# Performance work log

Measured on AMD Instinct MI355X. Metric: run time of the kernel, lower is better.

Reference implementation:

```python
import jax, jax.numpy as jnp
import numpy as np

NUM_CLASSES = 80
SCORE_THRESH = 0.5
NMS_THRESH = 0.5
TOP_K = 200  # max candidates kept per (image, class) before greedy NMS


def setup_inputs() -> dict:
    key = jax.random.key(0)
    k1, k2, k3 = jax.random.split(key, 3)
    B, A, HW, C = 8, 3, 5776, NUM_CLASSES  # 608-input YOLOv4 P3 level: 76*76
    # well-formed boxes in [0,1]: x1y1 + positive wh
    xy = jax.random.uniform(k1, (B, A, HW, 2)) * 0.8
    wh = jax.random.uniform(k2, (B, A, HW, 2)) * 0.2 + 0.01
    boxes = jnp.concatenate([xy, xy + wh], axis=-1)
    scores = jax.random.uniform(k3, (B, A, HW, C))
    return {"boxes": boxes, "scores": scores}


def _pairwise_iou(b):
    # b: [K, 4] (x1, y1, x2, y2) -> IoU matrix [K, K] (union mode)
    x1, y1, x2, y2 = b[:, 0], b[:, 1], b[:, 2], b[:, 3]
    area = (x2 - x1) * (y2 - y1)
    xx1 = jnp.maximum(x1[:, None], x1[None, :])
    yy1 = jnp.maximum(y1[:, None], y1[None, :])
    xx2 = jnp.minimum(x2[:, None], x2[None, :])
    yy2 = jnp.minimum(y2[:, None], y2[None, :])
    inter = jnp.maximum(0.0, xx2 - xx1) * jnp.maximum(0.0, yy2 - yy1)
    return inter / (area[:, None] + area[None, :] - inter)


def _nms_one(boxes, scores):
    # boxes: [N, 4], scores: [N] -> top-K candidates with greedy-NMS keep mask
    s = jnp.where(scores > SCORE_THRESH, scores, -jnp.inf)  # score threshold filter
    top_s, idx = jax.lax.top_k(s, TOP_K)                    # descending, like argsort()[::-1]
    b = boxes[idx]                                          # [K, 4]
    valid = jnp.isfinite(top_s)
    iou = _pairwise_iou(b)                                  # [K, K]

    def body(keep, i):
        # if box i survives, suppress all lower-scored boxes with IoU > thresh
        sup = keep[i] & (iou[i] > NMS_THRESH) & (jnp.arange(TOP_K) > i)
        return keep & ~sup, None

    keep, _ = jax.lax.scan(body, valid, jnp.arange(TOP_K))
    return b, top_s, keep


def reference(boxes, scores):
    B, A, HW, _ = boxes.shape
    C = scores.shape[-1]
    b = boxes.reshape(B, A * HW, 4)
    s = scores.reshape(B, A * HW, C)
    per_img = jax.vmap(lambda bb, ss: jax.vmap(_nms_one, in_axes=(None, 1))(bb, ss))
    boxes_k, scores_k, keep = per_img(b, s)  # [B,C,K,4], [B,C,K], [B,C,K]
    cls = jnp.broadcast_to(jnp.arange(C, dtype=boxes.dtype)[None, :, None], keep.shape)
    out_box = jnp.where(keep[..., None], boxes_k, 0.0)
    out_score = jnp.where(keep, scores_k, 0.0)
    out_cls = jnp.where(keep, cls, 0.0)
    # padded detections [B, C, K, 6] = (x1, y1, x2, y2, score, class_id)
    return jnp.concatenate([out_box, out_score[..., None], out_cls[..., None]], axis=-1)
```

## Files before the change

### kernel.cpp

```cpp
#include <hip/hip_runtime.h>
#include <stdint.h>

#define B_IMG  8
#define NANCH  17328
#define NCLS   80
#define TOPK   200
#define NTHR   256
#define NTHRB  512
#define CHUNK  64
#define NCHK   ((NANCH + CHUNK - 1) / CHUNK)
#define NCHKP  272
#define SLOT   12
#define NPOS   (NCHK * SLOT)
#define NBC    (B_IMG * NCLS)
#define THRESH_HI 0.98f

__device__ __forceinline__ void hist_add(float s, unsigned int* hist) {
  if (s > 0.5f) {
    unsigned int bin = (__float_as_uint(s) - 0x3F000000u) >> 15;
    if (bin > 255u) bin = 255u;
    atomicAdd(&hist[bin], 1u);
  }
}

__global__ __launch_bounds__(NTHR) void scatter_k(
    const float* __restrict__ scores,
    unsigned char* __restrict__ cnt2,
    unsigned long long* __restrict__ cand) {
  const int nb = blockIdx.x;
  const int b  = blockIdx.y;
  const int tid = threadIdx.x;
  const int wv = tid >> 6, lane = tid & 63;
  const int n0 = nb * CHUNK;

  __shared__ float tile[CHUNK][81];

  const int nrow = (NANCH - n0 < CHUNK) ? (NANCH - n0) : CHUNK;
  const int nf4 = nrow * (NCLS / 4);
  const float4* src4 = (const float4*)(scores + (size_t)(b * NANCH + n0) * NCLS);
  for (int f = tid; f < nf4; f += NTHR) {
    float4 v = src4[f];
    int n = f / 20, c4 = (f - n * 20) * 4;
    tile[n][c4] = v.x; tile[n][c4 + 1] = v.y;
    tile[n][c4 + 2] = v.z; tile[n][c4 + 3] = v.w;
  }
  __syncthreads();

  const bool rv = (lane < nrow);
  const unsigned long long lt = (1ull << lane) - 1ull;
  const int cbase = wv * 20;
#pragma unroll 4
  for (int cc = 0; cc < 20; ++cc) {
    const int c = cbase + cc;
    const int bc = b * NCLS + c;
    float s = rv ? tile[lane][c] : 0.f;
    const bool cd = (s > THRESH_HI);
    unsigned long long bal = __ballot(cd);
    if (cd) {
      unsigned int r = (unsigned int)__popcll(bal & lt);
      if (r < SLOT)
        cand[((size_t)bc * NCHK + nb) * SLOT + r] =
            ((unsigned long long)__float_as_uint(s) << 32) |
            (unsigned long long)(0xFFFFFFFFu - (unsigned int)(n0 + lane));
    }
    if (lane == 0)
      cnt2[(size_t)bc * NCHKP + nb] = (unsigned char)__popcll(bal);
  }
}

__global__ __launch_bounds__(NTHRB) void backend_k(
    const float* __restrict__ scores, const float* __restrict__ boxes,
    const unsigned char* __restrict__ cnt2, const unsigned long long* __restrict__ cand,
    float* __restrict__ out) {
  const int bc = blockIdx.x;
  const int b = bc / NCLS;
  const int c = bc - b * NCLS;
  const int tid = threadIdx.x;
  const int wv = tid >> 6, lane = tid & 63;
  const unsigned long long lt = (1ull << lane) - 1ull;

  __shared__ unsigned long long selk[512];
  __shared__ unsigned long long sorted[256];
  __shared__ unsigned int hist[256];
  __shared__ float sx1[256], sy1[256], sx2[256], sy2[256], sar[256], ssc[256];
  __shared__ int skeep[256];
  __shared__ __align__(16) unsigned long long sup[TOPK][4];
  __shared__ __align__(16) float eout[TOPK * 6];
  __shared__ unsigned int sh_cutbits;
  __shared__ int sh_sel, sh_bad;

  if (tid < 256) sorted[tid] = 0ull;
  if (tid == 0) { sh_sel = 0; sh_bad = 0; }
  __syncthreads();

  const unsigned long long* cb0 = cand + (size_t)bc * NCHK * SLOT;
  const unsigned char* ct0 = cnt2 + (size_t)bc * NCHKP;
  for (int p = tid; p < NPOS; p += NTHRB) {
    const int ch = p / SLOT;
    const int sl = p - ch * SLOT;
    unsigned int ci = (unsigned int)ct0[ch];
    if (sl == 0 && ci > SLOT) sh_bad = 1;
    unsigned long long k = 0ull;
    bool pred = (sl < (int)ci);
    if (pred) k = cb0[p];
    unsigned long long bal = __ballot(pred);
    if (bal) {
      int base0 = 0;
      if (lane == 0) base0 = atomicAdd(&sh_sel, (int)__popcll(bal));
      base0 = __shfl(base0, 0, 64);
      if (pred) {
        int pos = base0 + (int)__popcll(bal & lt);
        if (pos < 512) selk[pos] = k;
      }
    }
  }
  __syncthreads();

  int Msel = sh_sel;
  const bool fb = (sh_bad != 0) || (Msel < TOPK) || (Msel > 512);

  if (fb) {
    if (tid < 256) hist[tid] = 0u;
    if (tid == 0) sh_sel = 0;
    __syncthreads();
    const float* src = scores + (size_t)b * NANCH * NCLS + c;
    for (int i = tid; i < NANCH; i += NTHRB) hist_add(src[(size_t)i * NCLS], hist);
    __syncthreads();
    if (tid == 0) {
      unsigned int acc = 0;
      int cut = 0;
      for (int bin = 255; bin >= 0; --bin) {
        acc += hist[bin];
        if (acc >= TOPK) { cut = bin; break; }
      }
      sh_cutbits = 0x3F000000u + ((unsigned int)cut << 15);
    }
    __syncthreads();
    const unsigned int cutbits = sh_cutbits;
    for (int i = tid; i < NANCH; i += NTHRB) {
      float s = src[(size_t)i * NCLS];
      if (s > 0.5f && __float_as_uint(s) >= cutbits) {
        int slot = atomicAdd(&sh_sel, 1);
        if (slot < 512)
          selk[slot] = ((unsigned long long)__float_as_uint(s) << 32) |
                       (unsigned long long)(0xFFFFFFFFu - (unsigned int)i);
      }
    }
    __syncthreads();
    Msel = sh_sel; if (Msel > 512) Msel = 512;
  }

  if (tid < Msel) {
    const unsigned long long mk = selk[tid];
    int r = 0;
#pragma unroll 8
    for (int j = 0; j < Msel; ++j) r += (selk[j] > mk) ? 1 : 0;
    if (r < 256) sorted[r] = mk;
  }
  __syncthreads();

  if (tid < 256) {
    unsigned long long key = sorted[tid];
    int valid = (tid < TOPK) && (key != 0ull);
    unsigned int idx = 0xFFFFFFFFu - (unsigned int)(key & 0xFFFFFFFFull);
    float4 bx = make_float4(0.f, 0.f, 0.f, 0.f);
    if (valid) bx = ((const float4*)boxes)[(size_t)b * NANCH + idx];
    sx1[tid] = bx.x; sy1[tid] = bx.y; sx2[tid] = bx.z; sy2[tid] = bx.w;
    sar[tid] = __fmul_rn(bx.z - bx.x, bx.w - bx.y);
    ssc[tid] = valid ? __uint_as_float((unsigned int)(key >> 32)) : 0.f;
    skeep[tid] = valid;
  }
  __syncthreads();

  {
    float jx1[4], jy1[4], jx2[4], jy2[4], ja[4];
#pragma unroll
    for (int r = 0; r < 4; ++r) {
      int j = (r << 6) | lane;
      jx1[r] = sx1[j]; jy1[r] = sy1[j]; jx2[r] = sx2[j]; jy2[r] = sy2[j];
      ja[r] = sar[j];
    }
    float nx1 = sx1[wv], ny1 = sy1[wv], nx2 = sx2[wv], ny2 = sy2[wv], na = sar[wv];
    for (int k = 0; k < 25; ++k) {
      const int i = (k << 3) + wv;
      const float xi1 = nx1, yi1 = ny1, xi2 = nx2, yi2 = ny2, ai = na;
      const int inx = i + 8;
      if (inx < TOPK) {
        nx1 = sx1[inx]; ny1 = sy1[inx]; nx2 = sx2[inx]; ny2 = sy2[inx];
        na = sar[inx];
      }
      const int d = i >> 6;
      const int il = i & 63;
      unsigned long long dmask = (il == 63) ? 0ull : ((~0ull) << (il + 1));
      if (d == 3) dmask &= 0xFFull;
      unsigned long long w[4];
#pragma unroll
      for (int r = 0; r < 4; ++r) {
        unsigned long long word = 0ull;
        if ((r << 6) + 63 > i) {
          const unsigned long long wmask =
              (r > d) ? ((r == 3) ? 0xFFull : ~0ull) : dmask;
          float xx1 = fmaxf(xi1, jx1[r]);
          float yy1 = fmaxf(yi1, jy1[r]);
          float xx2 = fminf(xi2, jx2[r]);
          float yy2 = fminf(yi2, jy2[r]);
          float iw = fmaxf(0.f, __fsub_rn(xx2, xx1));
          float ih = fmaxf(0.f, __fsub_rn(yy2, yy1));
          float inter = __fmul_rn(iw, ih);
          float denom = __fsub_rn(__fadd_rn(ai, ja[r]), inter);
          float q = __fmul_rn(inter, __builtin_amdgcn_rcpf(denom));
          word = __ballot(q > 0.5f);
          unsigned long long gb = __ballot(fabsf(q - 0.5f) < 1e-5f) & wmask;
          if (gb)
            word = __ballot(__fdiv_rn(inter, denom) > 0.5f);
          word &= wmask;
        }
        w[r] = word;
      }
      if (lane == 0) {
        ulonglong2* dst = (ulonglong2*)&sup[i][0];
        ulonglong2 t0; t0.x = w[0]; t0.y = w[1];
        ulonglong2 t1; t1.x = w[2]; t1.y = w[3];
        dst[0] = t0; dst[1] = t1;
      }
    }
  }
  __syncthreads();

  if (tid < 64) {
    unsigned long long k0 = __ballot(skeep[tid] != 0);
    unsigned long long k1 = __ballot(skeep[64 + tid] != 0);
    unsigned long long k2 = __ballot(skeep[128 + tid] != 0);
    unsigned long long k3 = __ballot(skeep[192 + tid] != 0);
#define NMS_SCAN_WORD(KW, BASE, CNT)                                     \
    _Pragma("unroll 8")                                                  \
    for (int li = 0; li < (CNT); ++li) {                                 \
      const ulonglong2* s2p =                                            \
          reinterpret_cast<const ulonglong2*>(&sup[(BASE) + li][0]);     \
      ulonglong2 sa = s2p[0];                                            \
      ulonglong2 sb = s2p[1];                                            \
      unsigned long long m = 0ull - ((KW >> li) & 1ull);                 \
      k0 &= ~(sa.x & m); k1 &= ~(sa.y & m);                              \
      k2 &= ~(sb.x & m); k3 &= ~(sb.y & m);                              \
    }
    NMS_SCAN_WORD(k0, 0, 64)
    NMS_SCAN_WORD(k1, 64, 64)
    NMS_SCAN_WORD(k2, 128, 64)
    NMS_SCAN_WORD(k3, 192, 8)
#undef NMS_SCAN_WORD
    skeep[tid]        = (int)((k0 >> tid) & 1ull);
    skeep[64 + tid]   = (int)((k1 >> tid) & 1ull);
    skeep[128 + tid]  = (int)((k2 >> tid) & 1ull);
    skeep[192 + tid]  = (int)((k3 >> tid) & 1ull);
  }
  __syncthreads();

  if (tid < TOPK) {
    int kp = skeep[tid];
    eout[tid * 6 + 0] = kp ? sx1[tid] : 0.f;
    eout[tid * 6 + 1] = kp ? sy1[tid] : 0.f;
    eout[tid * 6 + 2] = kp ? sx2[tid] : 0.f;
    eout[tid * 6 + 3] = kp ? sy2[tid] : 0.f;
    eout[tid * 6 + 4] = kp ? ssc[tid] : 0.f;
    eout[tid * 6 + 5] = kp ? (float)c : 0.f;
  }
  __syncthreads();

  float4* out4 = (float4*)(out + (size_t)bc * (TOPK * 6));
  const float4* e4 = (const float4*)eout;
  for (int f = tid; f < (TOPK * 6) / 4; f += NTHRB) out4[f] = e4[f];
}

__global__ __launch_bounds__(NTHR) void select_nms_k(
    const float* __restrict__ boxes, const float* __restrict__ scores,
    float* __restrict__ out) {
  const int blk = blockIdx.x;
  const int b = blk / NCLS;
  const int c = blk - b * NCLS;
  const int tid = threadIdx.x;

  __shared__ unsigned int hist[256];
  __shared__ unsigned long long keys[1024];
  __shared__ float sx1[TOPK], sy1[TOPK], sx2[TOPK], sy2[TOPK], sar[TOPK], ssc[TOPK];
  __shared__ int skeep[TOPK];
  __shared__ unsigned int sh_cutbits;
  __shared__ int sh_m;

  const float* src = scores + (size_t)b * NANCH * NCLS + c;

  for (int j = tid; j < 256; j += NTHR) hist[j] = 0;
  if (tid == 0) sh_m = 0;
  __syncthreads();

  for (int i = tid; i < NANCH; i += NTHR) hist_add(src[(size_t)i * NCLS], hist);
  __syncthreads();

  if (tid == 0) {
    unsigned int acc = 0;
    int cut = 0;
    for (int bin = 255; bin >= 0; --bin) {
      acc += hist[bin];
      if (acc >= TOPK) { cut = bin; break; }
    }
    sh_cutbits = 0x3F000000u + ((unsigned int)cut << 15);
  }
  __syncthreads();
  const unsigned int cutbits = sh_cutbits;

  for (int i = tid; i < NANCH; i += NTHR) {
    float s = src[(size_t)i * NCLS];
    if (s > 0.5f && __float_as_uint(s) >= cutbits) {
      int slot = atomicAdd(&sh_m, 1);
      if (slot < 1024)
        keys[slot] = ((unsigned long long)__float_as_uint(s) << 32) |
                     (unsigned long long)(0xFFFFFFFFu - (unsigned int)i);
    }
  }
  __syncthreads();
  int M = sh_m; if (M > 1024) M = 1024;
  for (int j = M + tid; j < 1024; j += NTHR) keys[j] = 0ull;

  for (int size = 2; size <= 1024; size <<= 1) {
    for (int st = size >> 1; st > 0; st >>= 1) {
      __syncthreads();
      for (int t = tid; t < 512; t += NTHR) {
        int lo = 2 * t - (t & (st - 1));
        int hi = lo + st;
        bool desc = ((lo & size) == 0);
        unsigned long long a = keys[lo], bb = keys[hi];
        if ((a < bb) == desc) { keys[lo] = bb; keys[hi] = a; }
      }
    }
  }
  __syncthreads();

  if (tid < TOPK) {
    unsigned long long key = keys[tid];
    int valid = (key != 0ull);
    float sc = __uint_as_float((unsigned int)(key >> 32));
    unsigned int idx = 0xFFFFFFFFu - (unsigned int)(key & 0xFFFFFFFFull);
    float4 bx = make_float4(0.f, 0.f, 0.f, 0.f);
    if (valid) bx = ((const float4*)boxes)[(size_t)b * NANCH + idx];
    sx1[tid] = bx.x; sy1[tid] = bx.y; sx2[tid] = bx.z; sy2[tid] = bx.w;
    sar[tid] = __fmul_rn(bx.z - bx.x, bx.w - bx.y);
    ssc[tid] = valid ? sc : 0.f;
    skeep[tid] = valid;
  }
  __syncthreads();

  if (tid < 64) {
    const int lane = tid;
    float x1v[4], y1v[4], x2v[4], y2v[4], av[4];
    int km = 0;
#pragma unroll
    for (int r = 0; r < 4; ++r) {
      int j = lane + (r << 6);
      if (j < TOPK) {
        x1v[r] = sx1[j]; y1v[r] = sy1[j]; x2v[r] = sx2[j]; y2v[r] = sy2[j];
        av[r] = sar[j];
        if (skeep[j]) km |= (1 << r);
      } else {
        x1v[r] = 0.f; y1v[r] = 0.f; x2v[r] = 0.f; y2v[r] = 0.f; av[r] = 0.f;
      }
    }
#pragma unroll
    for (int ri = 0; ri < 4; ++ri) {
      const int imax = (ri == 3) ? (TOPK - 192) : 64;
      for (int li = 0; li < imax; ++li) {
        const int i = (ri << 6) + li;
        int kmi = __shfl(km, li, 64);
        if (!((kmi >> ri) & 1)) continue;
        float xi1 = __shfl(x1v[ri], li, 64);
        float yi1 = __shfl(y1v[ri], li, 64);
        float xi2 = __shfl(x2v[ri], li, 64);
        float yi2 = __shfl(y2v[ri], li, 64);
        float ai  = __shfl(av[ri],  li, 64);
#pragma unroll
        for (int r = 0; r < 4; ++r) {
          int j = lane + (r << 6);
          if (j > i && j < TOPK && ((km >> r) & 1)) {
            float xx1 = fmaxf(xi1, x1v[r]);
            float yy1 = fmaxf(yi1, y1v[r]);
            float xx2 = fminf(xi2, x2v[r]);
            float yy2 = fminf(yi2, y2v[r]);
            float iw = fmaxf(0.f, __fsub_rn(xx2, xx1));
            float ih = fmaxf(0.f, __fsub_rn(yy2, yy1));
            float inter = __fmul_rn(iw, ih);
            float denom = __fsub_rn(__fadd_rn(ai, av[r]), inter);
            float iou = __fdiv_rn(inter, denom);
            if (iou > 0.5f) km &= ~(1 << r);
          }
        }
      }
    }
#pragma unroll
    for (int r = 0; r < 4; ++r) {
      int j = lane + (r << 6);
      if (j < TOPK) skeep[j] = (km >> r) & 1;
    }
  }
  __syncthreads();

  const size_t base = ((size_t)b * NCLS + c) * (TOPK * 6);
  for (int f = tid; f < TOPK * 6; f += NTHR) {
    int k = f / 6, comp = f - k * 6;
    float v = 0.f;
    if (skeep[k]) {
      switch (comp) {
        case 0: v = sx1[k]; break;
        case 1: v = sy1[k]; break;
        case 2: v = sx2[k]; break;
        case 3: v = sy2[k]; break;
        case 4: v = ssc[k]; break;
        default: v = (float)c; break;
      }
    }
    out[base + f] = v;
  }
}

extern "C" void kernel_launch(void* const* d_in, const int* in_sizes, int n_in,
                              void* d_out, int out_size, void* d_ws, size_t ws_size,
                              hipStream_t stream) {
  (void)in_sizes; (void)n_in; (void)out_size;
  const float* boxes  = (const float*)d_in[0];
  const float* scores = (const float*)d_in[1];
  float* out = (float*)d_out;

  const size_t need_c2 = (size_t)NBC * NCHKP;
  const size_t need_cd = (size_t)NBC * NCHK * SLOT * sizeof(uint64_t);
  const size_t need = need_c2 + need_cd;

  if (ws_size >= need) {
    char* w = (char*)d_ws;
    unsigned char* cnt2      = (unsigned char*)w;       w += need_c2;
    unsigned long long* cand = (unsigned long long*)w;

    scatter_k<<<dim3(NCHK, B_IMG), NTHR, 0, stream>>>(scores, cnt2, cand);
    backend_k<<<NBC, NTHRB, 0, stream>>>(scores, boxes, cnt2, cand, out);
  } else {
    select_nms_k<<<NBC, NTHR, 0, stream>>>(boxes, scores, out);
  }
}
```

Baseline: 72.95 us.

## Split backend into select and NMS kernels with bitonic sort and division-free IoU test

New measurement: 79.71 us. +9.3%, slower.

```diff
diff --git a/kernel.cpp b/kernel.cpp
--- a/kernel.cpp
+++ b/kernel.cpp
@@ -68,34 +68,28 @@
   }
 }
 
-__global__ __launch_bounds__(NTHRB) void backend_k(
+__global__ __launch_bounds__(NTHR) void select_k(
     const float* __restrict__ scores, const float* __restrict__ boxes,
     const unsigned char* __restrict__ cnt2, const unsigned long long* __restrict__ cand,
-    float* __restrict__ out) {
+    float4* __restrict__ stagedBox, unsigned long long* __restrict__ stagedKey) {
   const int bc = blockIdx.x;
   const int b = bc / NCLS;
   const int c = bc - b * NCLS;
   const int tid = threadIdx.x;
-  const int wv = tid >> 6, lane = tid & 63;
+  const int lane = tid & 63;
   const unsigned long long lt = (1ull << lane) - 1ull;
 
   __shared__ unsigned long long selk[512];
-  __shared__ unsigned long long sorted[256];
   __shared__ unsigned int hist[256];
-  __shared__ float sx1[256], sy1[256], sx2[256], sy2[256], sar[256], ssc[256];
-  __shared__ int skeep[256];
-  __shared__ __align__(16) unsigned long long sup[TOPK][4];
-  __shared__ __align__(16) float eout[TOPK * 6];
   __shared__ unsigned int sh_cutbits;
   __shared__ int sh_sel, sh_bad;
 
-  if (tid < 256) sorted[tid] = 0ull;
   if (tid == 0) { sh_sel = 0; sh_bad = 0; }
   __syncthreads();
 
   const unsigned long long* cb0 = cand + (size_t)bc * NCHK * SLOT;
   const unsigned char* ct0 = cnt2 + (size_t)bc * NCHKP;
-  for (int p = tid; p < NPOS; p += NTHRB) {
+  for (int p = tid; p < NPOS; p += NTHR) {
     const int ch = p / SLOT;
     const int sl = p - ch * SLOT;
     unsigned int ci = (unsigned int)ct0[ch];
@@ -124,7 +118,7 @@
     if (tid == 0) sh_sel = 0;
     __syncthreads();
     const float* src = scores + (size_t)b * NANCH * NCLS + c;
-    for (int i = tid; i < NANCH; i += NTHRB) hist_add(src[(size_t)i * NCLS], hist);
+    for (int i = tid; i < NANCH; i += NTHR) hist_add(src[(size_t)i * NCLS], hist);
     __syncthreads();
     if (tid == 0) {
       unsigned int acc = 0;
@@ -137,7 +131,7 @@
     }
     __syncthreads();
     const unsigned int cutbits = sh_cutbits;
-    for (int i = tid; i < NANCH; i += NTHRB) {
+    for (int i = tid; i < NANCH; i += NTHR) {
       float s = src[(size_t)i * NCLS];
       if (s > 0.5f && __float_as_uint(s) >= cutbits) {
         int slot = atomicAdd(&sh_sel, 1);
@@ -150,21 +144,51 @@
     Msel = sh_sel; if (Msel > 512) Msel = 512;
   }
 
-  if (tid < Msel) {
-    const unsigned long long mk = selk[tid];
-    int r = 0;
-#pragma unroll 8
-    for (int j = 0; j < Msel; ++j) r += (selk[j] > mk) ? 1 : 0;
-    if (r < 256) sorted[r] = mk;
-  }
-  __syncthreads();
-
-  if (tid < 256) {
-    unsigned long long key = sorted[tid];
+  const int S = (Msel <= 256) ? 256 : 512;
+  for (int j = Msel + tid; j < S; j += NTHR) selk[j] = 0ull;
+
+  for (int size = 2; size <= S; size <<= 1) {
+    for (int st = size >> 1; st > 0; st >>= 1) {
+      __syncthreads();
+      for (int t = tid; t < (S >> 1); t += NTHR) {
+        int lo = 2 * t - (t & (st - 1));
+        int hi = lo + st;
+        bool desc = ((lo & size) == 0);
+        unsigned long long a = selk[lo], bb = selk[hi];
+        if ((a < bb) == desc) { selk[lo] = bb; selk[hi] = a; }
+      }
+    }
+  }
+  __syncthreads();
+
+  {
+    unsigned long long key = selk[tid];
     int valid = (tid < TOPK) && (key != 0ull);
     unsigned int idx = 0xFFFFFFFFu - (unsigned int)(key & 0xFFFFFFFFull);
     float4 bx = make_float4(0.f, 0.f, 0.f, 0.f);
     if (valid) bx = ((const float4*)boxes)[(size_t)b * NANCH + idx];
+    stagedBox[(size_t)bc * 256 + tid] = bx;
+    stagedKey[(size_t)bc * 256 + tid] = valid ? key : 0ull;
+  }
+}
+
+__global__ __launch_bounds__(NTHRB) void nms_k(
+    const float4* __restrict__ stagedBox, const unsigned long long* __restrict__ stagedKey,
+    float* __restrict__ out) {
+  const int bc = blockIdx.x;
+  const int c = bc - (bc / NCLS) * NCLS;
+  const int tid = threadIdx.x;
+  const int wv = tid >> 6, lane = tid & 63;
+
+  __shared__ float sx1[256], sy1[256], sx2[256], sy2[256], sar[256], ssc[256];
+  __shared__ int skeep[256];
+  __shared__ __align__(16) unsigned long long sup[TOPK][4];
+  __shared__ __align__(16) float eout[TOPK * 6];
+
+  if (tid < 256) {
+    unsigned long long key = stagedKey[(size_t)bc * 256 + tid];
+    float4 bx = stagedBox[(size_t)bc * 256 + tid];
+    int valid = (tid < TOPK) && (key != 0ull);
     sx1[tid] = bx.x; sy1[tid] = bx.y; sx2[tid] = bx.z; sy2[tid] = bx.w;
     sar[tid] = __fmul_rn(bx.z - bx.x, bx.w - bx.y);
     ssc[tid] = valid ? __uint_as_float((unsigned int)(key >> 32)) : 0.f;
@@ -208,9 +232,11 @@
           float ih = fmaxf(0.f, __fsub_rn(yy2, yy1));
           float inter = __fmul_rn(iw, ih);
           float denom = __fsub_rn(__fadd_rn(ai, ja[r]), inter);
-          float q = __fmul_rn(inter, __builtin_amdgcn_rcpf(denom));
-          word = __ballot(q > 0.5f);
-          unsigned long long gb = __ballot(fabsf(q - 0.5f) < 1e-5f) & wmask;
+          float i2 = __fadd_rn(inter, inter);
+          word = __ballot(i2 > denom);
+          unsigned long long gb =
+              __ballot((i2 > denom) &&
+                       (i2 <= __fmul_rn(denom, 1.0000005f))) & wmask;
           if (gb)
             word = __ballot(__fdiv_rn(inter, denom) > 0.5f);
           word &= wmask;
@@ -429,15 +455,21 @@
 
   const size_t need_c2 = (size_t)NBC * NCHKP;
   const size_t need_cd = (size_t)NBC * NCHK * SLOT * sizeof(uint64_t);
-  const size_t need = need_c2 + need_cd;
+  const size_t need_sb = (size_t)NBC * 256 * sizeof(float4);
+  const size_t need_sk = (size_t)NBC * 256 * sizeof(uint64_t);
+  const size_t need = need_c2 + need_cd + need_sb + need_sk;
 
   if (ws_size >= need) {
     char* w = (char*)d_ws;
-    unsigned char* cnt2      = (unsigned char*)w;       w += need_c2;
-    unsigned long long* cand = (unsigned long long*)w;
+    unsigned char* cnt2           = (unsigned char*)w;       w += need_c2;
+    unsigned long long* cand      = (unsigned long long*)w;  w += need_cd;
+    float4* stagedBox             = (float4*)w;              w += need_sb;
+    unsigned long long* stagedKey = (unsigned long long*)w;
 
     scatter_k<<<dim3(NCHK, B_IMG), NTHR, 0, stream>>>(scores, cnt2, cand);
-    backend_k<<<NBC, NTHRB, 0, stream>>>(scores, boxes, cnt2, cand, out);
+    select_k<<<NBC, NTHR, 0, stream>>>(scores, boxes, cnt2, cand,
+                                       stagedBox, stagedKey);
+    nms_k<<<NBC, NTHRB, 0, stream>>>(stagedBox, stagedKey, out);
   } else {
     select_nms_k<<<NBC, NTHR, 0, stream>>>(boxes, scores, out);
   }
```

## Fuse IoU computation into serial NMS scan, bitonic sort, and 256-thread backend

Applied to the files above, without the earlier changes.

Result: slower. 98.53 us (+35.1%).

```diff
diff --git a/kernel.cpp b/kernel.cpp
--- a/kernel.cpp
+++ b/kernel.cpp
@@ -6,7 +6,6 @@
 #define NCLS   80
 #define TOPK   200
 #define NTHR   256
-#define NTHRB  512
 #define CHUNK  64
 #define NCHK   ((NANCH + CHUNK - 1) / CHUNK)
 #define NCHKP  272
@@ -68,7 +67,35 @@
   }
 }
 
-__global__ __launch_bounds__(NTHRB) void backend_k(
+#define DO_R(R, KR, EXTRA) {                                                  \
+    bool mk = (EXTRA);                                                        \
+    float xx1 = fmaxf(xi1, jx1[R]);                                           \
+    float yy1 = fmaxf(yi1, jy1[R]);                                           \
+    float xx2 = fminf(xi2, jx2[R]);                                           \
+    float yy2 = fminf(yi2, jy2[R]);                                           \
+    float iw = fmaxf(0.f, __fsub_rn(xx2, xx1));                               \
+    float ih = fmaxf(0.f, __fsub_rn(yy2, yy1));                               \
+    float inter = __fmul_rn(iw, ih);                                          \
+    float denom = __fsub_rn(__fadd_rn(ai, ja[R]), inter);                     \
+    float i2 = __fadd_rn(inter, inter);                    \
+    bool s = mk && (i2 > denom);                                              \
+    bool gbp = s && (i2 <= __fmul_rn(denom, 1.0000005f));                     \
+    if (__ballot(gbp)) {                     \
+      if (gbp) s = __fdiv_rn(inter, denom) > 0.5f;                            \
+    }                                                                         \
+    KR &= ~__ballot(s);                                                       \
+  }
+
+#define ROW_D(D, KD, ILMAX, ...)                                              \
+  for (int il = 0; il < (ILMAX); ++il) {                                      \
+    if (!((KD >> il) & 1ull)) continue;     \
+    const int i = 64 * (D) + il;                                              \
+    const float xi1 = sx1[i], yi1 = sy1[i], xi2 = sx2[i],                     \
+                yi2 = sy2[i], ai = sar[i];                                    \
+    __VA_ARGS__                                                               \
+  }
+
+__global__ __launch_bounds__(NTHR) void backend_k(
     const float* __restrict__ scores, const float* __restrict__ boxes,
     const unsigned char* __restrict__ cnt2, const unsigned long long* __restrict__ cand,
     float* __restrict__ out) {
@@ -76,26 +103,23 @@
   const int b = bc / NCLS;
   const int c = bc - b * NCLS;
   const int tid = threadIdx.x;
-  const int wv = tid >> 6, lane = tid & 63;
+  const int lane = tid & 63;
   const unsigned long long lt = (1ull << lane) - 1ull;
 
   __shared__ unsigned long long selk[512];
-  __shared__ unsigned long long sorted[256];
   __shared__ unsigned int hist[256];
   __shared__ float sx1[256], sy1[256], sx2[256], sy2[256], sar[256], ssc[256];
   __shared__ int skeep[256];
-  __shared__ __align__(16) unsigned long long sup[TOPK][4];
   __shared__ __align__(16) float eout[TOPK * 6];
   __shared__ unsigned int sh_cutbits;
   __shared__ int sh_sel, sh_bad;
 
-  if (tid < 256) sorted[tid] = 0ull;
   if (tid == 0) { sh_sel = 0; sh_bad = 0; }
   __syncthreads();
 
   const unsigned long long* cb0 = cand + (size_t)bc * NCHK * SLOT;
   const unsigned char* ct0 = cnt2 + (size_t)bc * NCHKP;
-  for (int p = tid; p < NPOS; p += NTHRB) {
+  for (int p = tid; p < NPOS; p += NTHR) {
     const int ch = p / SLOT;
     const int sl = p - ch * SLOT;
     unsigned int ci = (unsigned int)ct0[ch];
@@ -124,7 +148,7 @@
     if (tid == 0) sh_sel = 0;
     __syncthreads();
     const float* src = scores + (size_t)b * NANCH * NCLS + c;
-    for (int i = tid; i < NANCH; i += NTHRB) hist_add(src[(size_t)i * NCLS], hist);
+    for (int i = tid; i < NANCH; i += NTHR) hist_add(src[(size_t)i * NCLS], hist);
     __syncthreads();
     if (tid == 0) {
       unsigned int acc = 0;
@@ -137,7 +161,7 @@
     }
     __syncthreads();
     const unsigned int cutbits = sh_cutbits;
-    for (int i = tid; i < NANCH; i += NTHRB) {
+    for (int i = tid; i < NANCH; i += NTHR) {
       float s = src[(size_t)i * NCLS];
       if (s > 0.5f && __float_as_uint(s) >= cutbits) {
         int slot = atomicAdd(&sh_sel, 1);
@@ -150,17 +174,25 @@
     Msel = sh_sel; if (Msel > 512) Msel = 512;
   }
 
-  if (tid < Msel) {
-    const unsigned long long mk = selk[tid];
-    int r = 0;
-#pragma unroll 8
-    for (int j = 0; j < Msel; ++j) r += (selk[j] > mk) ? 1 : 0;
-    if (r < 256) sorted[r] = mk;
-  }
-  __syncthreads();
-
-  if (tid < 256) {
-    unsigned long long key = sorted[tid];
+  const int S = (Msel <= 256) ? 256 : 512;
+  for (int j = Msel + tid; j < S; j += NTHR) selk[j] = 0ull;
+
+  for (int size = 2; size <= S; size <<= 1) {
+    for (int st = size >> 1; st > 0; st >>= 1) {
+      __syncthreads();
+      for (int t = tid; t < (S >> 1); t += NTHR) {
+        int lo = 2 * t - (t & (st - 1));
+        int hi = lo + st;
+        bool desc = ((lo & size) == 0);
+        unsigned long long a = selk[lo], bb = selk[hi];
+        if ((a < bb) == desc) { selk[lo] = bb; selk[hi] = a; }
+      }
+    }
+  }
+  __syncthreads();
+
+  {
+    unsigned long long key = selk[tid];
     int valid = (tid < TOPK) && (key != 0ull);
     unsigned int idx = 0xFFFFFFFFu - (unsigned int)(key & 0xFFFFFFFFull);
     float4 bx = make_float4(0.f, 0.f, 0.f, 0.f);
@@ -172,7 +204,12 @@
   }
   __syncthreads();
 
-  {
+  if (tid < 64) {
+    unsigned long long k0 = __ballot(skeep[lane] != 0);
+    unsigned long long k1 = __ballot(skeep[64 + lane] != 0);
+    unsigned long long k2 = __ballot(skeep[128 + lane] != 0);
+    unsigned long long k3 = __ballot(skeep[192 + lane] != 0);
+
     float jx1[4], jy1[4], jx2[4], jy2[4], ja[4];
 #pragma unroll
     for (int r = 0; r < 4; ++r) {
@@ -180,78 +217,26 @@
       jx1[r] = sx1[j]; jy1[r] = sy1[j]; jx2[r] = sx2[j]; jy2[r] = sy2[j];
       ja[r] = sar[j];
     }
-    float nx1 = sx1[wv], ny1 = sy1[wv], nx2 = sx2[wv], ny2 = sy2[wv], na = sar[wv];
-    for (int k = 0; k < 25; ++k) {
-      const int i = (k << 3) + wv;
-      const float xi1 = nx1, yi1 = ny1, xi2 = nx2, yi2 = ny2, ai = na;
-      const int inx = i + 8;
-      if (inx < TOPK) {
-        nx1 = sx1[inx]; ny1 = sy1[inx]; nx2 = sx2[inx]; ny2 = sy2[inx];
-        na = sar[inx];
-      }
-      const int d = i >> 6;
-      const int il = i & 63;
-      unsigned long long dmask = (il == 63) ? 0ull : ((~0ull) << (il + 1));
-      if (d == 3) dmask &= 0xFFull;
-      unsigned long long w[4];
-#pragma unroll
-      for (int r = 0; r < 4; ++r) {
-        unsigned long long word = 0ull;
-        if ((r << 6) + 63 > i) {
-          const unsigned long long wmask =
-              (r > d) ? ((r == 3) ? 0xFFull : ~0ull) : dmask;
-          float xx1 = fmaxf(xi1, jx1[r]);
-          float yy1 = fmaxf(yi1, jy1[r]);
-          float xx2 = fminf(xi2, jx2[r]);
-          float yy2 = fminf(yi2, jy2[r]);
-          float iw = fmaxf(0.f, __fsub_rn(xx2, xx1));
-          float ih = fmaxf(0.f, __fsub_rn(yy2, yy1));
-          float inter = __fmul_rn(iw, ih);
-          float denom = __fsub_rn(__fadd_rn(ai, ja[r]), inter);
-          float q = __fmul_rn(inter, __builtin_amdgcn_rcpf(denom));
-          word = __ballot(q > 0.5f);
-          unsigned long long gb = __ballot(fabsf(q - 0.5f) < 1e-5f) & wmask;
-          if (gb)
-            word = __ballot(__fdiv_rn(inter, denom) > 0.5f);
-          word &= wmask;
-        }
-        w[r] = word;
-      }
-      if (lane == 0) {
-        ulonglong2* dst = (ulonglong2*)&sup[i][0];
-        ulonglong2 t0; t0.x = w[0]; t0.y = w[1];
-        ulonglong2 t1; t1.x = w[2]; t1.y = w[3];
-        dst[0] = t0; dst[1] = t1;
-      }
-    }
-  }
-  __syncthreads();
-
-  if (tid < 64) {
-    unsigned long long k0 = __ballot(skeep[tid] != 0);
-    unsigned long long k1 = __ballot(skeep[64 + tid] != 0);
-    unsigned long long k2 = __ballot(skeep[128 + tid] != 0);
-    unsigned long long k3 = __ballot(skeep[192 + tid] != 0);
-#define NMS_SCAN_WORD(KW, BASE, CNT)                                     \
-    _Pragma("unroll 8")                                                  \
-    for (int li = 0; li < (CNT); ++li) {                                 \
-      const ulonglong2* s2p =                                            \
-          reinterpret_cast<const ulonglong2*>(&sup[(BASE) + li][0]);     \
-      ulonglong2 sa = s2p[0];                                            \
-      ulonglong2 sb = s2p[1];                                            \
-      unsigned long long m = 0ull - ((KW >> li) & 1ull);                 \
-      k0 &= ~(sa.x & m); k1 &= ~(sa.y & m);                              \
-      k2 &= ~(sb.x & m); k3 &= ~(sb.y & m);                              \
-    }
-    NMS_SCAN_WORD(k0, 0, 64)
-    NMS_SCAN_WORD(k1, 64, 64)
-    NMS_SCAN_WORD(k2, 128, 64)
-    NMS_SCAN_WORD(k3, 192, 8)
-#undef NMS_SCAN_WORD
-    skeep[tid]        = (int)((k0 >> tid) & 1ull);
-    skeep[64 + tid]   = (int)((k1 >> tid) & 1ull);
-    skeep[128 + tid]  = (int)((k2 >> tid) & 1ull);
-    skeep[192 + tid]  = (int)((k3 >> tid) & 1ull);
+
+    ROW_D(0, k0, 64,
+          DO_R(0, k0, lane > il)
+          DO_R(1, k1, true)
+          DO_R(2, k2, true)
+          DO_R(3, k3, lane < 8))
+    ROW_D(1, k1, 64,
+          DO_R(1, k1, lane > il)
+          DO_R(2, k2, true)
+          DO_R(3, k3, lane < 8))
+    ROW_D(2, k2, 64,
+          DO_R(2, k2, lane > il)
+          DO_R(3, k3, lane < 8))
+    ROW_D(3, k3, 8,
+          DO_R(3, k3, (lane > il) && (lane < 8)))
+
+    skeep[lane]        = (int)((k0 >> lane) & 1ull);
+    skeep[64 + lane]   = (int)((k1 >> lane) & 1ull);
+    skeep[128 + lane]  = (int)((k2 >> lane) & 1ull);
+    skeep[192 + lane]  = (int)((k3 >> lane) & 1ull);
   }
   __syncthreads();
 
@@ -268,7 +253,7 @@
 
   float4* out4 = (float4*)(out + (size_t)bc * (TOPK * 6));
   const float4* e4 = (const float4*)eout;
-  for (int f = tid; f < (TOPK * 6) / 4; f += NTHRB) out4[f] = e4[f];
+  for (int f = tid; f < (TOPK * 6) / 4; f += NTHR) out4[f] = e4[f];
 }
 
 __global__ __launch_bounds__(NTHR) void select_nms_k(
@@ -437,7 +422,7 @@
     unsigned long long* cand = (unsigned long long*)w;
 
     scatter_k<<<dim3(NCHK, B_IMG), NTHR, 0, stream>>>(scores, cnt2, cand);
-    backend_k<<<NBC, NTHRB, 0, stream>>>(scores, boxes, cnt2, cand, out);
+    backend_k<<<NBC, NTHR, 0, stream>>>(scores, boxes, cnt2, cand, out);
   } else {
     select_nms_k<<<NBC, NTHR, 0, stream>>>(boxes, scores, out);
   }
```
